# Kernel optimization log

Hardware: AMD Instinct MI355X
Metric: run time of the kernel (lower is better)

Reference implementation:

```python
import jax, jax.numpy as jnp
import numpy as np

B, H, D = 32, 64, 512          # batch, attn heads, head_dim (shared KV: V == K cache)
ROPE = 64                       # qk_rope_head_dim (partial rotary on last 64 dims)
HALF = ROPE // 2
NB, BS = 2048, 64               # paged cache: num blocks, block size
MB = NB // B                    # blocks per sequence
SMAX = MB * BS                  # 4096 max cached tokens per sequence
IH, ID = 64, 128                # indexer heads / head dim
TOPK = 512                      # index_topk
SCALE = 1.0 / float(np.sqrt(D))


def partial_rotary(x, cos, sin):
    # interleaved rope on the LAST ROPE dims (rope_dim_start = D - ROPE)
    x1, x2 = x[..., :D - ROPE], x[..., D - ROPE:]
    c = cos[:, None, :]  # [B,1,HALF] broadcast over heads
    s = sin[:, None, :]
    xe, xo = x2[..., 0::2], x2[..., 1::2]
    re = xe * c - xo * s
    ro = xe * s + xo * c
    rot = jnp.stack([re, ro], axis=-1).reshape(x2.shape)
    return jnp.concatenate([x1, rot], axis=-1)


def dyn_quant(x):
    # per-token dynamic int8 quant (kept in f32; values are exact int8 levels)
    scale = jnp.maximum(jnp.max(jnp.abs(x), axis=-1, keepdims=True), 1e-12) / 127.0
    scale = jnp.where(scale < 1e-6, 1.0, scale)
    xq = jnp.clip(jnp.round(x / scale), -128.0, 127.0)
    return xq, scale


def setup_inputs() -> dict:
    key = jax.random.key(0)
    ks = jax.random.split(key, 8)
    q = jax.random.normal(ks[0], (B, H, D), jnp.float32)
    cos = jax.random.normal(ks[1], (B, HALF), jnp.float32)
    sin = jax.random.normal(ks[2], (B, HALF), jnp.float32)
    kv_cache = jax.random.normal(ks[3], (NB, BS, D), jnp.float32)
    q_idx = jax.random.normal(ks[4], (B, IH, ID), jnp.float32)
    k_idx_cache = jax.random.normal(ks[5], (NB, BS, ID), jnp.float32)
    attn_sink = jax.random.normal(ks[6], (H,), jnp.float32) * 0.1
    block_tables = jnp.arange(B * MB, dtype=jnp.int32).reshape(B, MB)
    seq_lens = jax.random.randint(ks[7], (B,), 2 * TOPK, SMAX + 1, dtype=jnp.int32)
    return dict(q=q, cos=cos, sin=sin, kv_cache=kv_cache, q_idx=q_idx,
                k_idx_cache=k_idx_cache, attn_sink=attn_sink,
                block_tables=block_tables, seq_lens=seq_lens)


def reference(q, cos, sin, kv_cache, q_idx, k_idx_cache, attn_sink, block_tables, seq_lens):
    # 1) partial interleaved rotary on q's last ROPE dims
    qr = partial_rotary(q, cos, sin)
    # 2) paged gather of shared KV and indexer K caches
    k_all = kv_cache[block_tables].reshape(B, SMAX, D)      # [B,S,D]
    k_idx = k_idx_cache[block_tables].reshape(B, SMAX, ID)  # [B,S,ID]
    pos = jnp.arange(SMAX)
    valid = pos[None, :] < seq_lens[:, None]                # [B,S]
    # 3) int8 lightning indexer -> top-k token selection
    qq, qs = dyn_quant(q_idx)                               # [B,IH,ID],[B,IH,1]
    kq, kss = dyn_quant(k_idx)                              # [B,S,ID],[B,S,1]
    iscore = (jnp.einsum('bhd,bsd->bhs', qq, kq) * qs).sum(axis=1) * kss[..., 0]  # [B,S]
    iscore = jnp.where(valid, iscore, -jnp.inf)
    _, top_idx = jax.lax.top_k(iscore, TOPK)                # [B,TOPK]
    sel = jnp.zeros((B, SMAX), bool).at[jnp.arange(B)[:, None], top_idx].set(True)
    keep = (sel & valid) | (pos[None, :] == 0)              # sink token always attended
    # 4) sparse shared-KV attention (V = K), attn_sink added on first cached token
    scores = jnp.einsum('bhd,bsd->bhs', qr, k_all) * SCALE
    scores = scores.at[:, :, 0].add(attn_sink[None, :])
    scores = jnp.where(keep[:, None, :], scores, -jnp.inf)
    w = jax.nn.softmax(scores, axis=-1)
    out = jnp.einsum('bhs,bsd->bhd', w, k_all)              # [B,H,D]
    return out
```

## Files before the change

### kernel.cpp

```cpp
#include <hip/hip_runtime.h>
#include <math.h>

#define B_ 32
#define H_ 64
#define D_ 512
#define ROPE_ 64
#define HALF_ 32
#define NB_ 2048
#define BS_ 64
#define MB_ 64
#define SMAX_ 4096
#define IH_ 64
#define ID_ 128
#define TOPK_ 512
#define SEL_CAP_ 544
#define KB_ROWS_ 576
#define SCALE_ 0.044194173824159216f

typedef __bf16 bf16x8 __attribute__((ext_vector_type(8)));
typedef float f32x4 __attribute__((ext_vector_type(4)));

__device__ __forceinline__ unsigned short f2bf(float f) {
  unsigned u = __float_as_uint(f);
  u += 0x7FFFu + ((u >> 16) & 1u);
  return (unsigned short)(u >> 16);
}

#define BARSYNC()                                        \
  do {                                                   \
    asm volatile("s_waitcnt lgkmcnt(0)" ::: "memory");   \
    __builtin_amdgcn_s_barrier();                        \
  } while (0)

__global__ __launch_bounds__(64) void k_prep(
    const float* __restrict__ q, const float* __restrict__ cosb,
    const float* __restrict__ sinb, const float* __restrict__ q_idx,
    unsigned short* __restrict__ qrb, unsigned short* __restrict__ qqb,
    float* __restrict__ qs) {
  int r = blockIdx.x, t = threadIdx.x;
  if (r < B_ * H_) {
    const float* x = q + (size_t)r * D_;
    unsigned short* y = qrb + (size_t)r * D_;
    int b = r >> 6;
    unsigned pk[4];
    if (t < 56) {
      float4 v0 = ((const float4*)x)[t * 2];
      float4 v1 = ((const float4*)x)[t * 2 + 1];
      pk[0] = f2bf(v0.x) | ((unsigned)f2bf(v0.y) << 16);
      pk[1] = f2bf(v0.z) | ((unsigned)f2bf(v0.w) << 16);
      pk[2] = f2bf(v1.x) | ((unsigned)f2bf(v1.y) << 16);
      pk[3] = f2bf(v1.z) | ((unsigned)f2bf(v1.w) << 16);
      *(uint4*)(y + t * 8) = make_uint4(pk[0], pk[1], pk[2], pk[3]);
    } else {
      int p0 = (t - 56) * 4;
#pragma unroll
      for (int i = 0; i < 4; i++) {
        int p = p0 + i;
        float c = cosb[b * HALF_ + p], s = sinb[b * HALF_ + p];
        float xe = x[448 + 2 * p], xo = x[448 + 2 * p + 1];
        float re = xe * c - xo * s;
        float ro = xe * s + xo * c;
        pk[i] = f2bf(re) | ((unsigned)f2bf(ro) << 16);
      }
      *(uint4*)(y + 448 + 8 * (t - 56)) = make_uint4(pk[0], pk[1], pk[2], pk[3]);
    }
  } else {
    int rr = r - B_ * H_;
    const float* x = q_idx + (size_t)rr * ID_;
    float2 v = *(const float2*)(x + t * 2);
    float m = fmaxf(fabsf(v.x), fabsf(v.y));
#pragma unroll
    for (int off = 32; off; off >>= 1) m = fmaxf(m, __shfl_xor(m, off));
    float scale = fmaxf(m, 1e-12f) / 127.0f;
    if (scale < 1e-6f) scale = 1.0f;
    float q0 = fminf(fmaxf(rintf(v.x / scale), -128.0f), 127.0f);
    float q1 = fminf(fmaxf(rintf(v.y / scale), -128.0f), 127.0f);
    ((unsigned*)qqb)[rr * (ID_ / 2) + t] = f2bf(q0) | ((unsigned)f2bf(q1) << 16);
    if (t == 0) qs[rr] = scale;
  }
}

__global__ __launch_bounds__(256) void k_iscore(
    const float* __restrict__ k_idx_cache, const unsigned short* __restrict__ qqb,
    const float* __restrict__ qs, const int* __restrict__ block_tables,
    const int* __restrict__ seq_lens, float* __restrict__ iscore) {
  int m = blockIdx.x, b = blockIdx.y;
  int t = threadIdx.x, lane = t & 63, w = t >> 6;
  int s_base = m * BS_;
  int seq = seq_lens[b];
  float* out = iscore + (size_t)b * SMAX_ + s_base;
  if (s_base >= seq) {
    if (t < 64) out[t] = -INFINITY;
    return;
  }
  __shared__ __align__(16) unsigned short kq[64 * 136];
  __shared__ __align__(16) unsigned short qql[64 * 136];
  __shared__ float ksc[64];
  int phys = block_tables[b * MB_ + m];
  const float* krows = k_idx_cache + (size_t)phys * BS_ * ID_;
  int half = lane & 31, hw = lane >> 5;
  float4 vv[8];
#pragma unroll
  for (int rr = 0; rr < 8; rr++)
    vv[rr] = *(const float4*)(krows + (w * 16 + rr * 2 + hw) * ID_ + half * 4);
#pragma unroll
  for (int rr = 0; rr < 8; rr++) {
    int s = w * 16 + rr * 2 + hw;
    float4 v = vv[rr];
    float mx = fmaxf(fmaxf(fabsf(v.x), fabsf(v.y)), fmaxf(fabsf(v.z), fabsf(v.w)));
#pragma unroll
    for (int off = 1; off < 32; off <<= 1) mx = fmaxf(mx, __shfl_xor(mx, off));
    float scale = fmaxf(mx, 1e-12f) / 127.0f;
    if (scale < 1e-6f) scale = 1.0f;
    float q0 = fminf(fmaxf(rintf(v.x / scale), -128.0f), 127.0f);
    float q1 = fminf(fmaxf(rintf(v.y / scale), -128.0f), 127.0f);
    float q2 = fminf(fmaxf(rintf(v.z / scale), -128.0f), 127.0f);
    float q3 = fminf(fmaxf(rintf(v.w / scale), -128.0f), 127.0f);
    unsigned p0 = (unsigned)f2bf(q0) | ((unsigned)f2bf(q1) << 16);
    unsigned p1 = (unsigned)f2bf(q2) | ((unsigned)f2bf(q3) << 16);
    *(uint2*)((unsigned*)kq + s * 68 + half * 2) = make_uint2(p0, p1);
    if (half == 0) ksc[s] = scale;
  }
  const int4* qg = (const int4*)(qqb + (size_t)b * IH_ * ID_);
  for (int i = t; i < 64 * 16; i += 256) {
    int row = i >> 4, c = i & 15;
    *(int4*)((char*)qql + row * 272 + c * 16) = qg[row * 16 + c];
  }
  __syncthreads();
  int quad = lane >> 4, lr = lane & 15;
  float facc[4] = {0.f, 0.f, 0.f, 0.f};
  const float* qsrow = qs + b * IH_;
#pragma unroll
  for (int ht = 0; ht < 4; ht++) {
    f32x4 acc = {0.f, 0.f, 0.f, 0.f};
#pragma unroll
    for (int ks = 0; ks < 4; ks++) {
      bf16x8 a = *(const bf16x8*)(kq + (w * 16 + lr) * 136 + ks * 32 + quad * 8);
      bf16x8 bb = *(const bf16x8*)(qql + (ht * 16 + lr) * 136 + ks * 32 + quad * 8);
      acc = __builtin_amdgcn_mfma_f32_16x16x32_bf16(a, bb, acc, 0, 0, 0);
    }
    float qsv = qsrow[ht * 16 + lr];
#pragma unroll
    for (int r = 0; r < 4; r++) facc[r] += acc[r] * qsv;
  }
#pragma unroll
  for (int off = 1; off < 16; off <<= 1) {
#pragma unroll
    for (int r = 0; r < 4; r++) facc[r] += __shfl_xor(facc[r], off);
  }
  if (lr == 0) {
#pragma unroll
    for (int r = 0; r < 4; r++) {
      int sl = w * 16 + quad * 4 + r;
      out[sl] = (s_base + sl < seq) ? facc[r] * ksc[sl] : -INFINITY;
    }
  }
}

__global__ __launch_bounds__(256) void k_topk(
    const float* __restrict__ iscore, int* __restrict__ keep_idx,
    int* __restrict__ keep_cnt) {
  int b = blockIdx.x, t = threadIdx.x;
  int lane = t & 63, w = t >> 6;
  __shared__ unsigned keys[SMAX_];
  __shared__ unsigned hist[4][256];
  __shared__ unsigned wtot[4];
  __shared__ unsigned sh_prefix, sh_remaining, sh_cnt;
  const float* row = iscore + (size_t)b * SMAX_;
  for (int i = t; i < SMAX_; i += 256) {
    unsigned u = __float_as_uint(row[i]);
    keys[i] = (u & 0x80000000u) ? ~u : (u | 0x80000000u);
  }
  if (t == 0) { sh_prefix = 0u; sh_remaining = TOPK_; sh_cnt = 0u; }
  hist[0][t] = 0u; hist[1][t] = 0u; hist[2][t] = 0u; hist[3][t] = 0u;
  __syncthreads();
  for (int pass = 0; pass < 4; pass++) {
    int shift = 24 - 8 * pass;
    unsigned prefix = sh_prefix;
    unsigned rem = sh_remaining;
    unsigned pmask = (pass == 0) ? 0u : (0xFFFFFFFFu << (shift + 8));
    for (int i = t; i < SMAX_; i += 256) {
      unsigned k = keys[i];
      if ((k & pmask) == prefix) atomicAdd(&hist[w][(k >> shift) & 255u], 1u);
    }
    __syncthreads();
    unsigned cnt_t = hist[0][t] + hist[1][t] + hist[2][t] + hist[3][t];
    hist[0][t] = 0u; hist[1][t] = 0u; hist[2][t] = 0u; hist[3][t] = 0u;
    unsigned v = cnt_t;
#pragma unroll
    for (int off = 1; off < 64; off <<= 1) {
      unsigned o = __shfl_down(v, off);
      if (lane + off < 64) v += o;
    }
    if (lane == 0) wtot[w] = v;
    __syncthreads();
    unsigned tail = 0;
    for (int w2 = w + 1; w2 < 4; w2++) tail += wtot[w2];
    unsigned S = v + tail;
    if (S >= rem && S - cnt_t < rem) {
      sh_prefix = prefix | ((unsigned)t << shift);
      sh_remaining = rem - (S - cnt_t);
    }
    __syncthreads();
  }
  unsigned K = sh_prefix, R = sh_remaining;
  int* kidx = keep_idx + b * SEL_CAP_;
  for (int i = t; i < SMAX_; i += 256) {
    if (keys[i] > K) {
      unsigned p = atomicAdd(&sh_cnt, 1u);
      kidx[p] = i;
    }
  }
  int lo = t * 16;
  unsigned ec = 0;
#pragma unroll
  for (int j = 0; j < 16; j++) ec += (keys[lo + j] == K) ? 1u : 0u;
  unsigned pv = ec;
#pragma unroll
  for (int off = 1; off < 64; off <<= 1) {
    unsigned o = __shfl_up(pv, off);
    if (lane >= off) pv += o;
  }
  if (lane == 63) wtot[w] = pv;
  __syncthreads();
  unsigned base_eq = 0;
  for (int w2 = 0; w2 < w; w2++) base_eq += wtot[w2];
  unsigned rank = base_eq + pv - ec;
  unsigned G = sh_cnt;
  for (int j = 0; j < 16; j++) {
    if (keys[lo + j] == K) {
      if (rank < R) kidx[G + rank] = lo + j;
      rank++;
    }
  }
  __syncthreads();
  bool kept0 = (keys[0] >= K);
  int cnt = kept0 ? TOPK_ : (TOPK_ + 1);
  if (t == 0) {
    if (!kept0) kidx[TOPK_] = 0;
    keep_cnt[b] = cnt;
  }
  for (int i = cnt + t; i < SEL_CAP_; i += 256) kidx[i] = 0;
}

__global__ __launch_bounds__(256) void k_scores(
    const float* __restrict__ kv_cache, const unsigned short* __restrict__ qrb,
    const float* __restrict__ attn_sink, const int* __restrict__ block_tables,
    const int* __restrict__ keep_idx, const int* __restrict__ keep_cnt,
    float* __restrict__ scores, unsigned short* __restrict__ kb16) {
  int c = blockIdx.x, b = blockIdx.y;
  int t = threadIdx.x, lane = t & 63, w = t >> 6;
  int cnt = keep_cnt[b];
  int base = c * 32;
  int n = min(cnt - base, 32);
  unsigned short* kbrow = kb16 + (size_t)(b * KB_ROWS_ + base) * D_;
  if (n <= 0) {
    for (int i = t; i < 32 * 32; i += 256) {
      int row = i >> 5, x = i & 31;
      *(uint4*)(kbrow + (size_t)row * D_ + x * 16) = make_uint4(0u, 0u, 0u, 0u);
    }
    return;
  }
  __shared__ __align__(16) unsigned short kt[2][32 * 136];
  __shared__ int srow_off[32];
  __shared__ int sglb[32];
  const int* kidx = keep_idx + b * SEL_CAP_;
  if (t < 32) {
    int sg = (t < n) ? kidx[base + t] : 0;
    sglb[t] = (t < n) ? sg : -1;
    srow_off[t] = block_tables[b * MB_ + (sg >> 6)] * BS_ + (sg & 63);
  }
  int quad = lane >> 4, lr = lane & 15;
  bf16x8 qa[4][4];
  {
    const unsigned short* qrow = qrb + (size_t)(b * 64 + w * 16 + lr) * D_ + quad * 8;
#pragma unroll
    for (int dr = 0; dr < 4; dr++)
#pragma unroll
      for (int ks = 0; ks < 4; ks++)
        qa[dr][ks] = *(const bf16x8*)(qrow + dr * 128 + ks * 32);
  }
  __syncthreads();
  int prow = t >> 5, pd4 = t & 31;
  float4 pvA[4], pvB[4];
#pragma unroll
  for (int it = 0; it < 4; it++) {
    int row = prow + it * 8;
    pvA[it] = make_float4(0.f, 0.f, 0.f, 0.f);
    if (row < n)
      pvA[it] = *(const float4*)(kv_cache + (size_t)srow_off[row] * D_ + pd4 * 4);
  }
  f32x4 acc[2] = {};
#pragma unroll
  for (int dr = 0; dr < 4; dr++) {
    if (dr < 3) {
#pragma unroll
      for (int it = 0; it < 4; it++) {
        int row = prow + it * 8;
        pvB[it] = make_float4(0.f, 0.f, 0.f, 0.f);
        if (row < n)
          pvB[it] = *(const float4*)(kv_cache + (size_t)srow_off[row] * D_ +
                                     (dr + 1) * 128 + pd4 * 4);
      }
    }
    unsigned short* ktc = kt[dr & 1];
#pragma unroll
    for (int it = 0; it < 4; it++) {
      int row = prow + it * 8;
      float4 v = pvA[it];
      unsigned lo_ = f2bf(v.x) | ((unsigned)f2bf(v.y) << 16);
      unsigned hi_ = f2bf(v.z) | ((unsigned)f2bf(v.w) << 16);
      uint2 pk = make_uint2(lo_, hi_);
      *(uint2*)(ktc + row * 136 + pd4 * 4) = pk;
      *(uint2*)(kbrow + (size_t)row * D_ + dr * 128 + pd4 * 4) = pk;
    }
    BARSYNC();
#pragma unroll
    for (int ks = 0; ks < 4; ks++) {
#pragma unroll
      for (int st = 0; st < 2; st++) {
        bf16x8 bb = *(const bf16x8*)(ktc + (st * 16 + lr) * 136 + ks * 32 + quad * 8);
        acc[st] = __builtin_amdgcn_mfma_f32_16x16x32_bf16(qa[dr][ks], bb, acc[st], 0, 0, 0);
      }
    }
#pragma unroll
    for (int it = 0; it < 4; it++) pvA[it] = pvB[it];
  }
#pragma unroll
  for (int st = 0; st < 2; st++) {
    int col = st * 16 + lr;
    if (col < n) {
      int sg = sglb[col];
#pragma unroll
      for (int r = 0; r < 4; r++) {
        int h = w * 16 + quad * 4 + r;
        float v = acc[st][r] * SCALE_;
        if (sg == 0) v += attn_sink[h];
        scores[((size_t)b * 64 + h) * SEL_CAP_ + base + col] = v;
      }
    }
  }
}

__global__ __launch_bounds__(64) void k_softmax(
    const int* __restrict__ keep_cnt, float* __restrict__ scores,
    unsigned short* __restrict__ wbf) {
  int r = blockIdx.x, t = threadIdx.x;
  int b = r >> 6;
  int cnt = keep_cnt[b];
  float* row = scores + (size_t)r * SEL_CAP_;
  float mx = -INFINITY;
  for (int i = t; i < cnt; i += 64) mx = fmaxf(mx, row[i]);
#pragma unroll
  for (int off = 32; off; off >>= 1) mx = fmaxf(mx, __shfl_xor(mx, off));
  float sum = 0.f;
  for (int i = t; i < cnt; i += 64) {
    float e = __expf(row[i] - mx);
    row[i] = e;
    sum += e;
  }
#pragma unroll
  for (int off = 32; off; off >>= 1) sum += __shfl_xor(sum, off);
  float inv = 1.0f / sum;
  unsigned short* wr = wbf + (size_t)r * SEL_CAP_;
  for (int i = t; i < SEL_CAP_; i += 64) {
    float v = (i < cnt) ? row[i] * inv : 0.f;
    wr[i] = f2bf(v);
  }
}

__global__ __launch_bounds__(256) void k_pv(
    const unsigned short* __restrict__ kb16, const unsigned short* __restrict__ wbf,
    float* __restrict__ out) {
  int dc = blockIdx.x, b = blockIdx.y;
  int t = threadIdx.x, lane = t & 63, w = t >> 6;
  __shared__ __align__(16) unsigned short ktr[2][64 * 72];
  int quad = lane >> 4, lr = lane & 15;
  f32x4 acc[4] = {};
  const unsigned short* kbb = kb16 + (size_t)b * KB_ROWS_ * D_ + dc * 64;
  const unsigned short* wrow = wbf + (size_t)(b * 64 + w * 16 + lr) * SEL_CAP_;
  bf16x8 wa[17];
#pragma unroll
  for (int j = 0; j < 17; j++) wa[j] = *(const bf16x8*)(wrow + j * 32 + quad * 8);
  int psg2 = t >> 4, pd4 = t & 15;
  ushort4 paA[2][2], paB[2][2];
#pragma unroll
  for (int it = 0; it < 2; it++) {
    int sg2 = psg2 + it * 16;
    int s0 = sg2 * 2;
    paA[it][0] = *(const ushort4*)(kbb + (size_t)s0 * D_ + pd4 * 4);
    paA[it][1] = *(const ushort4*)(kbb + (size_t)(s0 + 1) * D_ + pd4 * 4);
  }
#pragma unroll
  for (int sc = 0; sc < 9; sc++) {
    int width = (sc < 8) ? 64 : 32;
    if (sc < 8) {
      int nw = ((sc + 1) < 8) ? 64 : 32;
#pragma unroll
      for (int it = 0; it < 2; it++) {
        int sg2 = psg2 + it * 16;
        if (sg2 < (nw >> 1)) {
          int s0 = (sc + 1) * 64 + sg2 * 2;
          paB[it][0] = *(const ushort4*)(kbb + (size_t)s0 * D_ + pd4 * 4);
          paB[it][1] = *(const ushort4*)(kbb + (size_t)(s0 + 1) * D_ + pd4 * 4);
        }
      }
    }
    unsigned* kw = (unsigned*)ktr[sc & 1];
#pragma unroll
    for (int it = 0; it < 2; it++) {
      int sg2 = psg2 + it * 16;
      if (sg2 < (width >> 1)) {
        ushort4 a0 = paA[it][0], a1 = paA[it][1];
        kw[(pd4 * 4 + 0) * 36 + sg2] = (unsigned)a0.x | ((unsigned)a1.x << 16);
        kw[(pd4 * 4 + 1) * 36 + sg2] = (unsigned)a0.y | ((unsigned)a1.y << 16);
        kw[(pd4 * 4 + 2) * 36 + sg2] = (unsigned)a0.z | ((unsigned)a1.z << 16);
        kw[(pd4 * 4 + 3) * 36 + sg2] = (unsigned)a0.w | ((unsigned)a1.w << 16);
      }
    }
    BARSYNC();
    const unsigned short* ktc = ktr[sc & 1];
    int ksteps = width >> 5;
#pragma unroll
    for (int ks = 0; ks < 2; ks++) {
      if (ks < ksteps) {
        bf16x8 a = wa[sc * 2 + ks];
#pragma unroll
        for (int nt = 0; nt < 4; nt++) {
          bf16x8 bb = *(const bf16x8*)(ktc + (nt * 16 + lr) * 72 + ks * 32 + quad * 8);
          acc[nt] = __builtin_amdgcn_mfma_f32_16x16x32_bf16(a, bb, acc[nt], 0, 0, 0);
        }
      }
    }
#pragma unroll
    for (int it = 0; it < 2; it++) { paA[it][0] = paB[it][0]; paA[it][1] = paB[it][1]; }
  }
#pragma unroll
  for (int nt = 0; nt < 4; nt++) {
#pragma unroll
    for (int r = 0; r < 4; r++) {
      int h = w * 16 + quad * 4 + r;
      int d = dc * 64 + nt * 16 + lr;
      out[((size_t)b * 64 + h) * D_ + d] = acc[nt][r];
    }
  }
}

extern "C" void kernel_launch(void* const* d_in, const int* in_sizes, int n_in,
                              void* d_out, int out_size, void* d_ws, size_t ws_size,
                              hipStream_t stream) {
  (void)in_sizes; (void)n_in; (void)out_size; (void)ws_size;
  const float* q = (const float*)d_in[0];
  const float* cosb = (const float*)d_in[1];
  const float* sinb = (const float*)d_in[2];
  const float* kv_cache = (const float*)d_in[3];
  const float* q_idx = (const float*)d_in[4];
  const float* k_idx = (const float*)d_in[5];
  const float* sink = (const float*)d_in[6];
  const int* btab = (const int*)d_in[7];
  const int* slen = (const int*)d_in[8];
  float* out = (float*)d_out;
  char* ws = (char*)d_ws;
  unsigned short* qrb = (unsigned short*)(ws + 0);
  unsigned short* qqb = (unsigned short*)(ws + 2097152);
  float* qs = (float*)(ws + 2621440);
  float* iscore = (float*)(ws + 2629632);
  int* keep_idx = (int*)(ws + 3141632);
  int* keep_cnt = (int*)(ws + 3211264);
  float* scores = (float*)(ws + 3212288);
  unsigned short* wbf = (unsigned short*)(ws + 7668736);
  unsigned short* kb16 = (unsigned short*)(ws + 9896960);

  k_prep<<<dim3(4096), dim3(64), 0, stream>>>(q, cosb, sinb, q_idx, qrb, qqb, qs);
  k_iscore<<<dim3(64, 32), dim3(256), 0, stream>>>(k_idx, qqb, qs, btab, slen, iscore);
  k_topk<<<dim3(32), dim3(256), 0, stream>>>(iscore, keep_idx, keep_cnt);
  k_scores<<<dim3(17, 32), dim3(256), 0, stream>>>(kv_cache, qrb, sink, btab, keep_idx, keep_cnt, scores, kb16);
  k_softmax<<<dim3(2048), dim3(64), 0, stream>>>(keep_cnt, scores, wbf);
  k_pv<<<dim3(8, 32), dim3(256), 0, stream>>>(kb16, wbf, out);
}
```

Baseline: 403.6 us.

## Fuse softmax into PV kernel, aggregate radix histogram atomics, and trim LDS staging

Removes the separate softmax kernel: each PV block recomputes the row max, sum and bf16 weights directly from the fp32 scores, which saves a launch and the intermediate weight buffer at the cost of reading the scores three times per dc block. The top-k histogram uses ballot-based peer aggregation so that only one lane per distinct digit issues an LDS atomic. The iscore kernel reads quantized q directly from global memory instead of staging it in LDS. The scores kernel issues all kv loads up front instead of double-buffering them and adds an occupancy hint, and the zero-fill path for empty chunks now clears the full row width. The PV grid is remapped to a 1D launch with a swizzled batch/dc order.

```diff
diff --git a/kernel.cpp b/kernel.cpp
--- a/kernel.cpp
+++ b/kernel.cpp
@@ -24,6 +24,13 @@
   unsigned u = __float_as_uint(f);
   u += 0x7FFFu + ((u >> 16) & 1u);
   return (unsigned short)(u >> 16);
+}
+
+__device__ __forceinline__ bf16x8 pack_bf16x8(unsigned p0, unsigned p1,
+                                              unsigned p2, unsigned p3) {
+  union { uint4 u; bf16x8 v; } c;
+  c.u = make_uint4(p0, p1, p2, p3);
+  return c.v;
 }
 
 #define BARSYNC()                                        \
@@ -94,7 +101,6 @@
     return;
   }
   __shared__ __align__(16) unsigned short kq[64 * 136];
-  __shared__ __align__(16) unsigned short qql[64 * 136];
   __shared__ float ksc[64];
   int phys = block_tables[b * MB_ + m];
   const float* krows = k_idx_cache + (size_t)phys * BS_ * ID_;
@@ -121,22 +127,18 @@
     *(uint2*)((unsigned*)kq + s * 68 + half * 2) = make_uint2(p0, p1);
     if (half == 0) ksc[s] = scale;
   }
-  const int4* qg = (const int4*)(qqb + (size_t)b * IH_ * ID_);
-  for (int i = t; i < 64 * 16; i += 256) {
-    int row = i >> 4, c = i & 15;
-    *(int4*)((char*)qql + row * 272 + c * 16) = qg[row * 16 + c];
-  }
   __syncthreads();
   int quad = lane >> 4, lr = lane & 15;
   float facc[4] = {0.f, 0.f, 0.f, 0.f};
   const float* qsrow = qs + b * IH_;
+  const unsigned short* qgb = qqb + (size_t)b * IH_ * ID_;
 #pragma unroll
   for (int ht = 0; ht < 4; ht++) {
     f32x4 acc = {0.f, 0.f, 0.f, 0.f};
 #pragma unroll
     for (int ks = 0; ks < 4; ks++) {
       bf16x8 a = *(const bf16x8*)(kq + (w * 16 + lr) * 136 + ks * 32 + quad * 8);
-      bf16x8 bb = *(const bf16x8*)(qql + (ht * 16 + lr) * 136 + ks * 32 + quad * 8);
+      bf16x8 bb = *(const bf16x8*)(qgb + (ht * 16 + lr) * ID_ + ks * 32 + quad * 8);
       acc = __builtin_amdgcn_mfma_f32_16x16x32_bf16(a, bb, acc, 0, 0, 0);
     }
     float qsv = qsrow[ht * 16 + lr];
@@ -181,7 +183,19 @@
     unsigned pmask = (pass == 0) ? 0u : (0xFFFFFFFFu << (shift + 8));
     for (int i = t; i < SMAX_; i += 256) {
       unsigned k = keys[i];
-      if ((k & pmask) == prefix) atomicAdd(&hist[w][(k >> shift) & 255u], 1u);
+      bool act = ((k & pmask) == prefix);
+      unsigned long long amask = __ballot(act);
+      if (act) {
+        unsigned d = (k >> shift) & 255u;
+        unsigned long long peers = amask;
+#pragma unroll
+        for (int bit = 0; bit < 8; bit++) {
+          unsigned long long bb = __ballot((d >> bit) & 1u);
+          peers &= ((d >> bit) & 1u) ? bb : ~bb;
+        }
+        if ((__ffsll((unsigned long long)peers) - 1) == lane)
+          atomicAdd(&hist[w][d], (unsigned)__popcll(peers));
+      }
     }
     __syncthreads();
     unsigned cnt_t = hist[0][t] + hist[1][t] + hist[2][t] + hist[3][t];
@@ -243,7 +257,7 @@
   for (int i = cnt + t; i < SEL_CAP_; i += 256) kidx[i] = 0;
 }
 
-__global__ __launch_bounds__(256) void k_scores(
+__global__ __launch_bounds__(256, 2) void k_scores(
     const float* __restrict__ kv_cache, const unsigned short* __restrict__ qrb,
     const float* __restrict__ attn_sink, const int* __restrict__ block_tables,
     const int* __restrict__ keep_idx, const int* __restrict__ keep_cnt,
@@ -255,9 +269,9 @@
   int n = min(cnt - base, 32);
   unsigned short* kbrow = kb16 + (size_t)(b * KB_ROWS_ + base) * D_;
   if (n <= 0) {
-    for (int i = t; i < 32 * 32; i += 256) {
-      int row = i >> 5, x = i & 31;
-      *(uint4*)(kbrow + (size_t)row * D_ + x * 16) = make_uint4(0u, 0u, 0u, 0u);
+    for (int i = t; i < 32 * 64; i += 256) {
+      int row = i >> 6, x = i & 63;
+      *(uint4*)(kbrow + (size_t)row * D_ + x * 8) = make_uint4(0u, 0u, 0u, 0u);
     }
     return;
   }
@@ -282,32 +296,26 @@
   }
   __syncthreads();
   int prow = t >> 5, pd4 = t & 31;
-  float4 pvA[4], pvB[4];
-#pragma unroll
-  for (int it = 0; it < 4; it++) {
-    int row = prow + it * 8;
-    pvA[it] = make_float4(0.f, 0.f, 0.f, 0.f);
-    if (row < n)
-      pvA[it] = *(const float4*)(kv_cache + (size_t)srow_off[row] * D_ + pd4 * 4);
-  }
-  f32x4 acc[2] = {};
+  float4 pv[4][4];
 #pragma unroll
   for (int dr = 0; dr < 4; dr++) {
-    if (dr < 3) {
-#pragma unroll
-      for (int it = 0; it < 4; it++) {
-        int row = prow + it * 8;
-        pvB[it] = make_float4(0.f, 0.f, 0.f, 0.f);
-        if (row < n)
-          pvB[it] = *(const float4*)(kv_cache + (size_t)srow_off[row] * D_ +
-                                     (dr + 1) * 128 + pd4 * 4);
-      }
-    }
-    unsigned short* ktc = kt[dr & 1];
 #pragma unroll
     for (int it = 0; it < 4; it++) {
       int row = prow + it * 8;
-      float4 v = pvA[it];
+      float4 v = make_float4(0.f, 0.f, 0.f, 0.f);
+      if (row < n)
+        v = *(const float4*)(kv_cache + (size_t)srow_off[row] * D_ + dr * 128 + pd4 * 4);
+      pv[dr][it] = v;
+    }
+  }
+  f32x4 acc[2] = {};
+#pragma unroll
+  for (int dr = 0; dr < 4; dr++) {
+    unsigned short* ktc = kt[dr & 1];
+#pragma unroll
+    for (int it = 0; it < 4; it++) {
+      int row = prow + it * 8;
+      float4 v = pv[dr][it];
       unsigned lo_ = f2bf(v.x) | ((unsigned)f2bf(v.y) << 16);
       unsigned hi_ = f2bf(v.z) | ((unsigned)f2bf(v.w) << 16);
       uint2 pk = make_uint2(lo_, hi_);
@@ -323,8 +331,6 @@
         acc[st] = __builtin_amdgcn_mfma_f32_16x16x32_bf16(qa[dr][ks], bb, acc[st], 0, 0, 0);
       }
     }
-#pragma unroll
-    for (int it = 0; it < 4; it++) pvA[it] = pvB[it];
   }
 #pragma unroll
   for (int st = 0; st < 2; st++) {
@@ -342,55 +348,71 @@
   }
 }
 
-__global__ __launch_bounds__(64) void k_softmax(
-    const int* __restrict__ keep_cnt, float* __restrict__ scores,
-    unsigned short* __restrict__ wbf) {
-  int r = blockIdx.x, t = threadIdx.x;
-  int b = r >> 6;
+__global__ __launch_bounds__(256) void k_pv(
+    const unsigned short* __restrict__ kb16, const float* __restrict__ scores,
+    const int* __restrict__ keep_cnt, float* __restrict__ out) {
+  int f = blockIdx.x;
+  int b = (f & 7) | ((f >> 6) << 3);
+  int dc = (f >> 3) & 7;
+  int t = threadIdx.x, lane = t & 63, w = t >> 6;
+  int quad = lane >> 4, lr = lane & 15;
   int cnt = keep_cnt[b];
-  float* row = scores + (size_t)r * SEL_CAP_;
-  float mx = -INFINITY;
-  for (int i = t; i < cnt; i += 64) mx = fmaxf(mx, row[i]);
-#pragma unroll
-  for (int off = 32; off; off >>= 1) mx = fmaxf(mx, __shfl_xor(mx, off));
-  float sum = 0.f;
-  for (int i = t; i < cnt; i += 64) {
-    float e = __expf(row[i] - mx);
-    row[i] = e;
-    sum += e;
-  }
-#pragma unroll
-  for (int off = 32; off; off >>= 1) sum += __shfl_xor(sum, off);
-  float inv = 1.0f / sum;
-  unsigned short* wr = wbf + (size_t)r * SEL_CAP_;
-  for (int i = t; i < SEL_CAP_; i += 64) {
-    float v = (i < cnt) ? row[i] * inv : 0.f;
-    wr[i] = f2bf(v);
-  }
-}
-
-__global__ __launch_bounds__(256) void k_pv(
-    const unsigned short* __restrict__ kb16, const unsigned short* __restrict__ wbf,
-    float* __restrict__ out) {
-  int dc = blockIdx.x, b = blockIdx.y;
-  int t = threadIdx.x, lane = t & 63, w = t >> 6;
   __shared__ __align__(16) unsigned short ktr[2][64 * 72];
-  int quad = lane >> 4, lr = lane & 15;
-  f32x4 acc[4] = {};
   const unsigned short* kbb = kb16 + (size_t)b * KB_ROWS_ * D_ + dc * 64;
-  const unsigned short* wrow = wbf + (size_t)(b * 64 + w * 16 + lr) * SEL_CAP_;
-  bf16x8 wa[17];
-#pragma unroll
-  for (int j = 0; j < 17; j++) wa[j] = *(const bf16x8*)(wrow + j * 32 + quad * 8);
   int psg2 = t >> 4, pd4 = t & 15;
   ushort4 paA[2][2], paB[2][2];
 #pragma unroll
   for (int it = 0; it < 2; it++) {
-    int sg2 = psg2 + it * 16;
-    int s0 = sg2 * 2;
+    int s0 = (psg2 + it * 16) * 2;
     paA[it][0] = *(const ushort4*)(kbb + (size_t)s0 * D_ + pd4 * 4);
     paA[it][1] = *(const ushort4*)(kbb + (size_t)(s0 + 1) * D_ + pd4 * 4);
   }
+  int hs = w * 16 + lr;
+  const float* srow = scores + ((size_t)b * 64 + hs) * SEL_CAP_ + quad * 8;
+  float mx = -INFINITY;
+#pragma unroll
+  for (int j = 0; j < 17; j++) {
+    int s0 = j * 32 + quad * 8;
+    float4 u0 = *(const float4*)(srow + j * 32);
+    float4 u1 = *(const float4*)(srow + j * 32 + 4);
+    float vv[8] = {u0.x, u0.y, u0.z, u0.w, u1.x, u1.y, u1.z, u1.w};
+#pragma unroll
+    for (int e = 0; e < 8; e++) mx = fmaxf(mx, (s0 + e < cnt) ? vv[e] : -INFINITY);
+  }
+  mx = fmaxf(mx, __shfl_xor(mx, 16));
+  mx = fmaxf(mx, __shfl_xor(mx, 32));
+  asm volatile("" ::: "memory");
+  float sum = 0.f;
+#pragma unroll
+  for (int j = 0; j < 17; j++) {
+    int s0 = j * 32 + quad * 8;
+    float4 u0 = *(const float4*)(srow + j * 32);
+    float4 u1 = *(const float4*)(srow + j * 32 + 4);
+    float vv[8] = {u0.x, u0.y, u0.z, u0.w, u1.x, u1.y, u1.z, u1.w};
+#pragma unroll
+    for (int e = 0; e < 8; e++) sum += (s0 + e < cnt) ? __expf(vv[e] - mx) : 0.f;
+  }
+  sum += __shfl_xor(sum, 16);
+  sum += __shfl_xor(sum, 32);
+  float inv = 1.0f / sum;
+  asm volatile("" ::: "memory");
+  bf16x8 wa[17];
+#pragma unroll
+  for (int j = 0; j < 17; j++) {
+    int s0 = j * 32 + quad * 8;
+    float4 u0 = *(const float4*)(srow + j * 32);
+    float4 u1 = *(const float4*)(srow + j * 32 + 4);
+    float vv[8] = {u0.x, u0.y, u0.z, u0.w, u1.x, u1.y, u1.z, u1.w};
+    unsigned pk[4];
+#pragma unroll
+    for (int p = 0; p < 4; p++) {
+      float e0 = (s0 + 2 * p < cnt) ? __expf(vv[2 * p] - mx) * inv : 0.f;
+      float e1 = (s0 + 2 * p + 1 < cnt) ? __expf(vv[2 * p + 1] - mx) * inv : 0.f;
+      pk[p] = (unsigned)f2bf(e0) | ((unsigned)f2bf(e1) << 16);
+    }
+    wa[j] = pack_bf16x8(pk[0], pk[1], pk[2], pk[3]);
+  }
+  f32x4 acc[4] = {};
 #pragma unroll
   for (int sc = 0; sc < 9; sc++) {
     int width = (sc < 8) ? 64 : 32;
@@ -468,13 +490,11 @@
   int* keep_idx = (int*)(ws + 3141632);
   int* keep_cnt = (int*)(ws + 3211264);
   float* scores = (float*)(ws + 3212288);
-  unsigned short* wbf = (unsigned short*)(ws + 7668736);
   unsigned short* kb16 = (unsigned short*)(ws + 9896960);
 
   k_prep<<<dim3(4096), dim3(64), 0, stream>>>(q, cosb, sinb, q_idx, qrb, qqb, qs);
   k_iscore<<<dim3(64, 32), dim3(256), 0, stream>>>(k_idx, qqb, qs, btab, slen, iscore);
   k_topk<<<dim3(32), dim3(256), 0, stream>>>(iscore, keep_idx, keep_cnt);
   k_scores<<<dim3(17, 32), dim3(256), 0, stream>>>(kv_cache, qrb, sink, btab, keep_idx, keep_cnt, scores, kb16);
-  k_softmax<<<dim3(2048), dim3(64), 0, stream>>>(keep_cnt, scores, wbf);
-  k_pv<<<dim3(8, 32), dim3(256), 0, stream>>>(kb16, wbf, out);
-}
+  k_pv<<<dim3(256), dim3(256), 0, stream>>>(kb16, scores, keep_cnt, out);
+}
```

Measured after the change: 423.6 us. 1.05x slower.
